# Kernel tuning notes

Measured on AMD Instinct MI355X. Metric: run time of the kernel, lower is better.

Reference implementation:

```python
import jax, jax.numpy as jnp
import numpy as np

B, N, D = 8, 1024, 256
H = 8
DH = D // H
R = 4          # relation types 0..3; adj value 4 = no relation
FF = 1024
EPS = 1e-5


def _lin(k, fan_in, shape):
    return jax.random.normal(k, shape, jnp.float32) * (1.0 / np.sqrt(fan_in))


def setup_inputs() -> dict:
    key = jax.random.key(0)
    ks = jax.random.split(key, 16)
    src = jax.random.normal(ks[0], (B, N, D), jnp.float32)
    adj_matrix = jax.random.randint(ks[1], (B, N, N), 0, 5, dtype=jnp.int32)
    Wq = _lin(ks[2], D, (D, D)); bq = jnp.zeros((D,), jnp.float32)
    Wk = _lin(ks[3], D, (D, D)); bk = jnp.zeros((D,), jnp.float32)
    Wv = _lin(ks[4], D, (R, D, D)); bv = jnp.zeros((R, D), jnp.float32)
    Wo = _lin(ks[5], D, (D, D)); bo = jnp.zeros((D,), jnp.float32)
    W1 = _lin(ks[6], D, (D, FF)); b1 = jnp.zeros((FF,), jnp.float32)
    W2 = _lin(ks[7], FF, (FF, D)); b2 = jnp.zeros((D,), jnp.float32)
    g1 = jnp.ones((D,), jnp.float32); beta1 = jnp.zeros((D,), jnp.float32)
    g2 = jnp.ones((D,), jnp.float32); beta2 = jnp.zeros((D,), jnp.float32)
    return dict(src=src, adj_matrix=adj_matrix, Wq=Wq, bq=bq, Wk=Wk, bk=bk,
                Wv=Wv, bv=bv, Wo=Wo, bo=bo, W1=W1, b1=b1, W2=W2, b2=b2,
                g1=g1, beta1=beta1, g2=g2, beta2=beta2)


def _ln(x, g, b):
    m = x.mean(-1, keepdims=True)
    v = ((x - m) ** 2).mean(-1, keepdims=True)
    return (x - m) * jax.lax.rsqrt(v + EPS) * g + b


def reference(src, adj_matrix, Wq, bq, Wk, bk, Wv, bv, Wo, bo, W1, b1, W2, b2, g1, beta1, g2, beta2):
    Bb, Nn, Dm = src.shape
    h, dh = H, Dm // H
    q = (src @ Wq + bq).reshape(Bb, Nn, h, dh).transpose(0, 2, 1, 3)  # (B,H,N,dh)
    k = (src @ Wk + bk).reshape(Bb, Nn, h, dh).transpose(0, 2, 1, 3)
    scores = jnp.einsum('bhid,bhjd->bhij', q, k) / np.sqrt(dh)
    attn = jax.nn.softmax(scores, axis=-1)                             # (B,H,N,N)
    out = jnp.zeros_like(q)
    for r in range(Wv.shape[0]):  # small fixed relation loop, matches module
        v_r = (src @ Wv[r] + bv[r]).reshape(Bb, Nn, h, dh).transpose(0, 2, 1, 3)
        mask = (adj_matrix == r)[:, None]                              # (B,1,N,N)
        out = out + jnp.einsum('bhij,bhjd->bhid', attn * mask, v_r)
    attn_out = out.transpose(0, 2, 1, 3).reshape(Bb, Nn, Dm) @ Wo + bo
    x = _ln(src + attn_out, g1, beta1)
    ff = jax.nn.gelu(x @ W1 + b1, approximate=False) @ W2 + b2
    return _ln(x + ff, g2, beta2)
```

## Files before the change

### kernel.cpp

```cpp
#include <hip/hip_runtime.h>
#include <hip/hip_bf16.h>
#include <cmath>

constexpr int CB  = 8;
constexpr int CN  = 1024;
constexpr int CD  = 256;
constexpr int CH  = 8;
constexpr int CDH = 32;
constexpr int CR  = 4;
constexpr int CFF = 1024;
constexpr float CEPS = 1e-5f;
constexpr size_t SZH = (size_t)CB * CH * CN * CDH;

#define MODE_QKV   0
#define MODE_OPROJ 1
#define MODE_FFN1  2
#define MODE_FFN2  3

typedef float v4f __attribute__((ext_vector_type(4)));
typedef short v8s __attribute__((ext_vector_type(8)));

static __device__ __forceinline__ short f2bf(float f) {
    unsigned u = __builtin_bit_cast(unsigned, f);
    u += 0x7fff + ((u >> 16) & 1);
    return (short)(u >> 16);
}

static __device__ __forceinline__ void async_copy16(const void* g, void* l) {
    __builtin_amdgcn_global_load_lds(
        (const __attribute__((address_space(1))) void*)g,
        (__attribute__((address_space(3))) void*)l, 16, 0, 0);
}

template<int BM, int BN, int MODE>
__global__ __launch_bounds__(256)
void gemm_mfma(const short* __restrict__ A, const short* __restrict__ Bw,
               const float* __restrict__ biasv, const float* __restrict__ add,
               void* __restrict__ dest, int M, int K, int Nw)
{
    constexpr int WTM = BM / 2, WTN = BN / 2;
    constexpr int TM = WTM / 16, TN = WTN / 16;
    __shared__ short As[2][BM * 32];
    __shared__ short Bs[2][BN * 32];

    const int t    = threadIdx.x;
    const int lane = t & 63;
    const int w    = t >> 6;
    const int quad = lane >> 4, l15 = lane & 15;
    const int wm = w >> 1, wn = w & 1;
    const int m0 = blockIdx.x * BM, n0 = blockIdx.y * BN;

    const int srow = lane >> 2;
    const int scol = (lane & 3) * 8;

    v4f acc[TM][TN];
    #pragma unroll
    for (int i = 0; i < TM; ++i)
        #pragma unroll
        for (int j = 0; j < TN; ++j) acc[i][j] = (v4f){0.f, 0.f, 0.f, 0.f};

    for (int kt = 0; kt < K; kt += 64) {
        __syncthreads();
        #pragma unroll
        for (int s = 0; s < 2; ++s) {
            #pragma unroll
            for (int u = 0; u < BM / 64; ++u) {
                const int e0 = (w * (BM / 64) + u) * 512;
                const int row = (e0 >> 5) + srow;
                async_copy16(A + (size_t)(m0 + row) * K + kt + s * 32 + scol, &As[s][e0]);
            }
            #pragma unroll
            for (int u = 0; u < BN / 64; ++u) {
                const int e0 = (w * (BN / 64) + u) * 512;
                const int row = (e0 >> 5) + srow;
                async_copy16(Bw + (size_t)(n0 + row) * K + kt + s * 32 + scol, &Bs[s][e0]);
            }
        }
        __syncthreads();

        #pragma unroll
        for (int s = 0; s < 2; ++s) {
            v8s af[TM], bfr[TN];
            #pragma unroll
            for (int i = 0; i < TM; ++i)
                af[i] = *(const v8s*)&As[s][(wm * WTM + i * 16 + l15) * 32 + quad * 8];
            #pragma unroll
            for (int j = 0; j < TN; ++j)
                bfr[j] = *(const v8s*)&Bs[s][(wn * WTN + j * 16 + l15) * 32 + quad * 8];
            #pragma unroll
            for (int i = 0; i < TM; ++i)
                #pragma unroll
                for (int j = 0; j < TN; ++j)
                    acc[i][j] = __builtin_amdgcn_mfma_f32_16x16x32_bf16(
                        af[i], bfr[j], acc[i][j], 0, 0, 0);
        }
    }

    #pragma unroll
    for (int i = 0; i < TM; ++i) {
        #pragma unroll
        for (int j = 0; j < TN; ++j) {
            const int mb = m0 + wm * WTM + i * 16 + quad * 4;
            const int n  = n0 + wn * WTN + j * 16 + l15;
            float vals[4];
            #pragma unroll
            for (int rr = 0; rr < 4; ++rr) vals[rr] = acc[i][j][rr] + biasv[n];

            if (MODE == MODE_QKV) {
                const int b = mb >> 10, ii0 = mb & 1023;
                if (n < 512) {
                    const int plane = n >> 8, nn = n & 255;
                    const int h = nn >> 5, d = nn & 31;
                    #pragma unroll
                    for (int rr = 0; rr < 4; ++rr)
                        ((short*)dest)[(size_t)plane * SZH +
                            (((size_t)(b * CH + h)) * CN + ii0 + rr) * CDH + d] =
                            f2bf(vals[rr]);
                } else {
                    const int r2 = (n - 512) >> 8, nn = (n - 512) & 255;
                    const int h = nn >> 5, d = nn & 31;
                    short4 sv;
                    sv.x = f2bf(vals[0]); sv.y = f2bf(vals[1]);
                    sv.z = f2bf(vals[2]); sv.w = f2bf(vals[3]);
                    *(short4*)&((short*)dest)[2 * SZH +
                        (((size_t)(r2 * 64 + b * CH + h)) * CDH + d) * CN + ii0] = sv;
                }
            } else if (MODE == MODE_OPROJ || MODE == MODE_FFN2) {
                #pragma unroll
                for (int rr = 0; rr < 4; ++rr) {
                    const size_t idx = (size_t)(mb + rr) * Nw + n;
                    ((float*)dest)[idx] = vals[rr] + add[idx];
                }
            } else {
                #pragma unroll
                for (int rr = 0; rr < 4; ++rr) {
                    const size_t idx = (size_t)(mb + rr) * Nw + n;
                    ((short*)dest)[idx] = f2bf(0.5f * vals[rr] *
                        (1.0f + erff(vals[rr] * 0.70710678118654752f)));
                }
            }
        }
    }
}

__global__ __launch_bounds__(256)
void prep(const int* __restrict__ adj, const float* __restrict__ src,
          const float* __restrict__ Wq, const float* __restrict__ Wk,
          const float* __restrict__ Wv, const float* __restrict__ Wo,
          const float* __restrict__ W1, const float* __restrict__ W2,
          const float* __restrict__ bq, const float* __restrict__ bk,
          const float* __restrict__ bv, const float* __restrict__ bo,
          const float* __restrict__ b1, const float* __restrict__ b2,
          unsigned char* __restrict__ adj8, short* __restrict__ src_bf,
          short* __restrict__ wqkvT, short* __restrict__ woT,
          short* __restrict__ w1T, short* __restrict__ w2T,
          float* __restrict__ bpack)
{
    const int bx = blockIdx.x, t = threadIdx.x;
    if (bx < 8192) {
        const int i = bx * 256 + t;
        const int4 vv = ((const int4*)adj)[i];
        uchar4 c;
        c.x = (unsigned char)vv.x; c.y = (unsigned char)vv.y;
        c.z = (unsigned char)vv.z; c.w = (unsigned char)vv.w;
        ((uchar4*)adj8)[i] = c;
    } else if (bx < 10240) {
        const int i = (bx - 8192) * 256 + t;
        const float4 v = ((const float4*)src)[i];
        short4 o;
        o.x = f2bf(v.x); o.y = f2bf(v.y); o.z = f2bf(v.z); o.w = f2bf(v.w);
        ((short4*)src_bf)[i] = o;
    } else if (bx < 11776) {
        const int idx = (bx - 10240) * 256 + t;
        const int n = idx >> 8, k = idx & 255;
        float v;
        if (n < 256)      v = Wq[k * 256 + n];
        else if (n < 512) v = Wk[k * 256 + (n - 256)];
        else { const int r = (n - 512) >> 8;
               v = Wv[((size_t)r * 256 + k) * 256 + ((n - 512) & 255)]; }
        wqkvT[idx] = f2bf(v);
    } else if (bx < 12032) {
        const int idx = (bx - 11776) * 256 + t;
        const int n = idx >> 8, k = idx & 255;
        woT[idx] = f2bf(Wo[k * 256 + n]);
    } else if (bx < 13056) {
        const int idx = (bx - 12032) * 256 + t;
        const int n = idx >> 8, k = idx & 255;
        w1T[idx] = f2bf(W1[k * 1024 + n]);
    } else if (bx < 14080) {
        const int idx = (bx - 13056) * 256 + t;
        const int n = idx >> 10, k = idx & 1023;
        w2T[idx] = f2bf(W2[k * 256 + n]);
    } else {
        const int idx = (bx - 14080) * 256 + t;
        float bvv;
        if (idx < 256)       bvv = bq[idx];
        else if (idx < 512)  bvv = bk[idx - 256];
        else if (idx < 1536) bvv = bv[idx - 512];
        else if (idx < 1792) bvv = bo[idx - 1536];
        else if (idx < 2816) bvv = b1[idx - 1792];
        else                 bvv = b2[idx - 2816];
        bpack[idx] = bvv;
    }
}

__global__ __launch_bounds__(256)
void attn_mfma(const short* __restrict__ qg, const short* __restrict__ kg,
               const short* __restrict__ vt, const unsigned char* __restrict__ adj8,
               short* __restrict__ outh)
{
    __shared__ __align__(16) short ks[64 * 32];
    __shared__ __align__(16) short vtile[4][32][72];
    __shared__ __align__(16) short ps[64][68];
    __shared__ __align__(16) unsigned char adjs[64][72];
    __shared__ int lut[64][4];

    const int t    = threadIdx.x;
    const int lane = t & 63;
    const int w    = t >> 6;
    const int quad = lane >> 4;
    const int l15  = lane & 15;
    const int i0   = blockIdx.x * 64;
    const int h    = blockIdx.y;
    const int b    = blockIdx.z;
    const int bhh  = b * CH + h;
    const size_t bh = (size_t)bhh;

    if (t < 64) {
        const int b0 = t & 7, b1 = t >> 3;
        #pragma unroll
        for (int r = 0; r < 4; ++r) {
            const int lo = (b0 == r) ? 0x0100 : 0x0c0c;
            const int hi = (b1 == r) ? 0x0302 : 0x0c0c;
            lut[t][r] = lo | (hi << 16);
        }
    }

    const v8s qfrag = *(const v8s*)&qg[(bh * CN + i0 + 16 * w + l15) * CDH + quad * 8];

    v4f oacc[2];
    oacc[0] = (v4f){0.f, 0.f, 0.f, 0.f};
    oacc[1] = (v4f){0.f, 0.f, 0.f, 0.f};
    float plsum[4] = {0.f, 0.f, 0.f, 0.f};

    const float cs = 0.25503480f;
    const int arow = 16 * w + l15;

    const int srow = lane >> 2;
    const int scol = (lane & 3) * 8;
    const int vd0  = lane >> 3;
    const int vc   = (lane & 7) * 8;
    const short* vplane = vt + (((size_t)(w * 64 + bhh)) * CDH) * CN;
    const int aro = t >> 2;
    const int aco = (t & 3) * 16;

    for (int jt = 0; jt < 16; ++jt) {
        const int j0 = jt * 64;
        __syncthreads();

        async_copy16(kg + (bh * CN + j0 + 16 * w + srow) * CDH + scol,
                     &ks[(16 * w + srow) * 32]);
        #pragma unroll
        for (int it = 0; it < 4; ++it) {
            const int d = vd0 + 8 * it;
            const v8s vv = *(const v8s*)&vplane[(size_t)d * CN + j0 + vc];
            *(v8s*)&vtile[w][d][vc] = vv;
        }
        const int4 av = *(const int4*)&adj8[((size_t)b * CN + i0 + aro) * CN + j0 + aco];
        *(int4*)&adjs[aro][aco] = av;
        __syncthreads();

        v4f sacc[4];
        #pragma unroll
        for (int jb = 0; jb < 4; ++jb) {
            const v8s kfrag = *(const v8s*)&ks[(16 * jb + l15) * 32 + quad * 8];
            sacc[jb] = __builtin_amdgcn_mfma_f32_16x16x32_bf16(
                qfrag, kfrag, (v4f){0.f, 0.f, 0.f, 0.f}, 0, 0, 0);
        }

        #pragma unroll
        for (int rr = 0; rr < 4; ++rr) {
            const int prow = 16 * w + quad * 4 + rr;
            float p[4];
            #pragma unroll
            for (int jb = 0; jb < 4; ++jb) p[jb] = exp2f(cs * sacc[jb][rr]);
            plsum[rr] += (p[0] + p[1]) + (p[2] + p[3]);
            #pragma unroll
            for (int jb = 0; jb < 4; ++jb)
                ps[prow][16 * jb + l15] = f2bf(p[jb]);
        }

        #pragma unroll
        for (int kb = 0; kb < 2; ++kb) {
            const int2 p0 = *(const int2*)&ps[arow][32 * kb + quad * 8];
            const int2 p1 = *(const int2*)&ps[arow][32 * kb + quad * 8 + 4];
            const int2 ab = *(const int2*)&adjs[arow][32 * kb + quad * 8];
            int pf[4][4];
            #pragma unroll
            for (int half = 0; half < 2; ++half) {
                const unsigned a = (unsigned)(half ? ab.y : ab.x);
                const int P0 = half ? p1.x : p0.x;
                const int P1 = half ? p1.y : p0.y;
                const int idxA = (a & 7) | ((a >> 5) & 0x38);
                const int idxB = ((a >> 16) & 7) | ((a >> 21) & 0x38);
                const int4 selA = *(const int4*)&lut[idxA][0];
                const int4 selB = *(const int4*)&lut[idxB][0];
                pf[0][half * 2 + 0] = __builtin_amdgcn_perm(P0, P0, selA.x);
                pf[1][half * 2 + 0] = __builtin_amdgcn_perm(P0, P0, selA.y);
                pf[2][half * 2 + 0] = __builtin_amdgcn_perm(P0, P0, selA.z);
                pf[3][half * 2 + 0] = __builtin_amdgcn_perm(P0, P0, selA.w);
                pf[0][half * 2 + 1] = __builtin_amdgcn_perm(P1, P1, selB.x);
                pf[1][half * 2 + 1] = __builtin_amdgcn_perm(P1, P1, selB.y);
                pf[2][half * 2 + 1] = __builtin_amdgcn_perm(P1, P1, selB.z);
                pf[3][half * 2 + 1] = __builtin_amdgcn_perm(P1, P1, selB.w);
            }
            #pragma unroll
            for (int r = 0; r < 4; ++r) {
                const v8s pfr = __builtin_bit_cast(v8s,
                    make_int4(pf[r][0], pf[r][1], pf[r][2], pf[r][3]));
                #pragma unroll
                for (int cb = 0; cb < 2; ++cb) {
                    const v8s vfrag = *(const v8s*)&vtile[r][16 * cb + l15][32 * kb + quad * 8];
                    oacc[cb] = __builtin_amdgcn_mfma_f32_16x16x32_bf16(
                        pfr, vfrag, oacc[cb], 0, 0, 0);
                }
            }
        }
    }

    #pragma unroll
    for (int rr = 0; rr < 4; ++rr) {
        float l = plsum[rr];
        #pragma unroll
        for (int off = 1; off < 16; off <<= 1) l += __shfl_xor(l, off);
        const float inv = 1.f / l;
        const int row = i0 + 16 * w + quad * 4 + rr;
        #pragma unroll
        for (int cb = 0; cb < 2; ++cb)
            outh[((size_t)b * CN + row) * CD + h * CDH + 16 * cb + l15] =
                f2bf(oacc[cb][rr] * inv);
    }
}

__global__ __launch_bounds__(256)
void ln_kernel(const float* __restrict__ in, const float* __restrict__ g,
               const float* __restrict__ be, float* __restrict__ out,
               short* __restrict__ outb)
{
    __shared__ float red[4];
    const int row = blockIdx.x;
    const int t = threadIdx.x;
    const float x = in[(size_t)row * CD + t];

    float s = x;
    #pragma unroll
    for (int off = 32; off > 0; off >>= 1) s += __shfl_xor(s, off);
    if ((t & 63) == 0) red[t >> 6] = s;
    __syncthreads();
    const float mean = (red[0] + red[1] + red[2] + red[3]) * (1.f / CD);
    __syncthreads();

    const float dx = x - mean;
    float s2 = dx * dx;
    #pragma unroll
    for (int off = 32; off > 0; off >>= 1) s2 += __shfl_xor(s2, off);
    if ((t & 63) == 0) red[t >> 6] = s2;
    __syncthreads();
    const float var = (red[0] + red[1] + red[2] + red[3]) * (1.f / CD);

    const float y = dx * rsqrtf(var + CEPS) * g[t] + be[t];
    out[(size_t)row * CD + t] = y;
    if (outb) outb[(size_t)row * CD + t] = f2bf(y);
}

extern "C" void kernel_launch(void* const* d_in, const int* in_sizes, int n_in,
                              void* d_out, int out_size, void* d_ws, size_t ws_size,
                              hipStream_t stream)
{
    const float* src = (const float*)d_in[0];
    const int*   adj = (const int*)d_in[1];
    const float* Wq  = (const float*)d_in[2];
    const float* bq  = (const float*)d_in[3];
    const float* Wk  = (const float*)d_in[4];
    const float* bk  = (const float*)d_in[5];
    const float* Wv  = (const float*)d_in[6];
    const float* bv  = (const float*)d_in[7];
    const float* Wo  = (const float*)d_in[8];
    const float* bo  = (const float*)d_in[9];
    const float* W1  = (const float*)d_in[10];
    const float* b1  = (const float*)d_in[11];
    const float* W2  = (const float*)d_in[12];
    const float* b2  = (const float*)d_in[13];
    const float* g1  = (const float*)d_in[14];
    const float* be1 = (const float*)d_in[15];
    const float* g2  = (const float*)d_in[16];
    const float* be2 = (const float*)d_in[17];
    float* out = (float*)d_out;

    char* wsb = (char*)d_ws;
    const size_t MB = (size_t)1 << 20;

    unsigned char* adj8 = (unsigned char*)(wsb);
    short* qkv_bf = (short*)(wsb + 8 * MB);
    short* src_bf = (short*)(wsb + 32 * MB);
    short* wqkvT  = (short*)(wsb + 36 * MB);
    short* woT    = (short*)(wsb + 36 * MB + 768 * 1024);
    short* w1T    = (short*)(wsb + 36 * MB + 896 * 1024);
    short* w2T    = (short*)(wsb + 36 * MB + 1408 * 1024);
    float* bpack  = (float*)(wsb + 36 * MB + 1920 * 1024);
    short* heads_bf = (short*)(wsb + 38 * MB);
    float* tmp1   = (float*)(wsb + 42 * MB);
    float* xres   = (float*)(wsb + 8 * MB);
    short* x_bf   = (short*)(wsb + 32 * MB);
    short* h1_bf  = (short*)(wsb + 16 * MB);
    float* tmp2   = tmp1;

    const int M = CB * CN;
    dim3 blk(256);

    prep<<<dim3(14092), blk, 0, stream>>>(adj, src, Wq, Wk, Wv, Wo, W1, W2,
        bq, bk, bv, bo, b1, b2, adj8, src_bf, wqkvT, woT, w1T, w2T, bpack);

    gemm_mfma<128, 128, MODE_QKV><<<dim3(M / 128, 1536 / 128), blk, 0, stream>>>(
        src_bf, wqkvT, bpack, nullptr, qkv_bf, M, CD, 1536);

    attn_mfma<<<dim3(CN / 64, CH, CB), blk, 0, stream>>>(
        qkv_bf, qkv_bf + SZH, qkv_bf + 2 * SZH, adj8, heads_bf);

    gemm_mfma<128, 64, MODE_OPROJ><<<dim3(M / 128, CD / 64), blk, 0, stream>>>(
        heads_bf, woT, bpack + 1536, src, tmp1, M, CD, CD);
    ln_kernel<<<dim3(M), blk, 0, stream>>>(tmp1, g1, be1, xres, x_bf);

    gemm_mfma<128, 128, MODE_FFN1><<<dim3(M / 128, CFF / 128), blk, 0, stream>>>(
        x_bf, w1T, bpack + 1792, nullptr, h1_bf, M, CD, CFF);
    gemm_mfma<128, 64, MODE_FFN2><<<dim3(M / 128, CD / 64), blk, 0, stream>>>(
        h1_bf, w2T, bpack + 2816, xres, tmp2, M, CFF, CD);
    ln_kernel<<<dim3(M), blk, 0, stream>>>(tmp2, g2, be2, out, nullptr);
}
```

Measured before the change: 256.2 us.

## Double-buffer GEMM K-loop and split V projection into transposed GEMM

```diff
diff --git a/kernel.cpp b/kernel.cpp
--- a/kernel.cpp
+++ b/kernel.cpp
@@ -12,10 +12,11 @@
 constexpr float CEPS = 1e-5f;
 constexpr size_t SZH = (size_t)CB * CH * CN * CDH;
 
-#define MODE_QKV   0
+#define MODE_QK    0
 #define MODE_OPROJ 1
 #define MODE_FFN1  2
 #define MODE_FFN2  3
+#define MODE_VT    4
 
 typedef float v4f __attribute__((ext_vector_type(4)));
 typedef short v8s __attribute__((ext_vector_type(8)));
@@ -59,41 +60,43 @@
         #pragma unroll
         for (int j = 0; j < TN; ++j) acc[i][j] = (v4f){0.f, 0.f, 0.f, 0.f};
 
-    for (int kt = 0; kt < K; kt += 64) {
+    const int NK = K >> 5;
+
+    auto stage = [&](int buf, int kt) {
+        #pragma unroll
+        for (int u = 0; u < BM / 64; ++u) {
+            const int e0 = (w * (BM / 64) + u) * 512;
+            const int row = (e0 >> 5) + srow;
+            async_copy16(A + (size_t)(m0 + row) * K + kt + scol, &As[buf][e0]);
+        }
+        #pragma unroll
+        for (int u = 0; u < BN / 64; ++u) {
+            const int e0 = (w * (BN / 64) + u) * 512;
+            const int row = (e0 >> 5) + srow;
+            async_copy16(Bw + (size_t)(n0 + row) * K + kt + scol, &Bs[buf][e0]);
+        }
+    };
+
+    stage(0, 0);
+
+    for (int it = 0; it < NK; ++it) {
         __syncthreads();
-        #pragma unroll
-        for (int s = 0; s < 2; ++s) {
-            #pragma unroll
-            for (int u = 0; u < BM / 64; ++u) {
-                const int e0 = (w * (BM / 64) + u) * 512;
-                const int row = (e0 >> 5) + srow;
-                async_copy16(A + (size_t)(m0 + row) * K + kt + s * 32 + scol, &As[s][e0]);
-            }
-            #pragma unroll
-            for (int u = 0; u < BN / 64; ++u) {
-                const int e0 = (w * (BN / 64) + u) * 512;
-                const int row = (e0 >> 5) + srow;
-                async_copy16(Bw + (size_t)(n0 + row) * K + kt + s * 32 + scol, &Bs[s][e0]);
-            }
-        }
-        __syncthreads();
-
-        #pragma unroll
-        for (int s = 0; s < 2; ++s) {
-            v8s af[TM], bfr[TN];
-            #pragma unroll
-            for (int i = 0; i < TM; ++i)
-                af[i] = *(const v8s*)&As[s][(wm * WTM + i * 16 + l15) * 32 + quad * 8];
+        if (it + 1 < NK) stage((it + 1) & 1, (it + 1) << 5);
+
+        const int buf = it & 1;
+        v8s af[TM], bfr[TN];
+        #pragma unroll
+        for (int i = 0; i < TM; ++i)
+            af[i] = *(const v8s*)&As[buf][(wm * WTM + i * 16 + l15) * 32 + quad * 8];
+        #pragma unroll
+        for (int j = 0; j < TN; ++j)
+            bfr[j] = *(const v8s*)&Bs[buf][(wn * WTN + j * 16 + l15) * 32 + quad * 8];
+        #pragma unroll
+        for (int i = 0; i < TM; ++i)
             #pragma unroll
             for (int j = 0; j < TN; ++j)
-                bfr[j] = *(const v8s*)&Bs[s][(wn * WTN + j * 16 + l15) * 32 + quad * 8];
-            #pragma unroll
-            for (int i = 0; i < TM; ++i)
-                #pragma unroll
-                for (int j = 0; j < TN; ++j)
-                    acc[i][j] = __builtin_amdgcn_mfma_f32_16x16x32_bf16(
-                        af[i], bfr[j], acc[i][j], 0, 0, 0);
-        }
+                acc[i][j] = __builtin_amdgcn_mfma_f32_16x16x32_bf16(
+                    af[i], bfr[j], acc[i][j], 0, 0, 0);
     }
 
     #pragma unroll
@@ -103,27 +106,33 @@
             const int mb = m0 + wm * WTM + i * 16 + quad * 4;
             const int n  = n0 + wn * WTN + j * 16 + l15;
             float vals[4];
-            #pragma unroll
-            for (int rr = 0; rr < 4; ++rr) vals[rr] = acc[i][j][rr] + biasv[n];
-
-            if (MODE == MODE_QKV) {
+            if (MODE == MODE_VT) {
+                #pragma unroll
+                for (int rr = 0; rr < 4; ++rr) vals[rr] = acc[i][j][rr] + biasv[mb + rr];
+            } else {
+                #pragma unroll
+                for (int rr = 0; rr < 4; ++rr) vals[rr] = acc[i][j][rr] + biasv[n];
+            }
+
+            if (MODE == MODE_QK) {
                 const int b = mb >> 10, ii0 = mb & 1023;
-                if (n < 512) {
-                    const int plane = n >> 8, nn = n & 255;
-                    const int h = nn >> 5, d = nn & 31;
-                    #pragma unroll
-                    for (int rr = 0; rr < 4; ++rr)
-                        ((short*)dest)[(size_t)plane * SZH +
-                            (((size_t)(b * CH + h)) * CN + ii0 + rr) * CDH + d] =
-                            f2bf(vals[rr]);
-                } else {
-                    const int r2 = (n - 512) >> 8, nn = (n - 512) & 255;
-                    const int h = nn >> 5, d = nn & 31;
-                    short4 sv;
-                    sv.x = f2bf(vals[0]); sv.y = f2bf(vals[1]);
-                    sv.z = f2bf(vals[2]); sv.w = f2bf(vals[3]);
-                    *(short4*)&((short*)dest)[2 * SZH +
-                        (((size_t)(r2 * 64 + b * CH + h)) * CDH + d) * CN + ii0] = sv;
+                const int plane = n >> 8, nn = n & 255;
+                const int h = nn >> 5, d = nn & 31;
+                #pragma unroll
+                for (int rr = 0; rr < 4; ++rr)
+                    ((short*)dest)[(size_t)plane * SZH +
+                        (((size_t)(b * CH + h)) * CN + ii0 + rr) * CDH + d] =
+                        f2bf(vals[rr]);
+            } else if (MODE == MODE_VT) {
+                const int b = n >> 10, ii = n & 1023;
+                #pragma unroll
+                for (int rr = 0; rr < 4; ++rr) {
+                    const int m = mb + rr;
+                    const int r2 = m >> 8, hd = m & 255;
+                    const int h = hd >> 5, d = hd & 31;
+                    ((short*)dest)[2 * SZH +
+                        (((size_t)(r2 * 64 + b * CH + h)) * CDH + d) * CN + ii] =
+                        f2bf(vals[rr]);
                 }
             } else if (MODE == MODE_OPROJ || MODE == MODE_FFN2) {
                 #pragma unroll
@@ -421,8 +430,10 @@
     prep<<<dim3(14092), blk, 0, stream>>>(adj, src, Wq, Wk, Wv, Wo, W1, W2,
         bq, bk, bv, bo, b1, b2, adj8, src_bf, wqkvT, woT, w1T, w2T, bpack);
 
-    gemm_mfma<128, 128, MODE_QKV><<<dim3(M / 128, 1536 / 128), blk, 0, stream>>>(
-        src_bf, wqkvT, bpack, nullptr, qkv_bf, M, CD, 1536);
+    gemm_mfma<128, 128, MODE_QK><<<dim3(M / 128, 4), blk, 0, stream>>>(
+        src_bf, wqkvT, bpack, nullptr, qkv_bf, M, CD, 512);
+    gemm_mfma<128, 128, MODE_VT><<<dim3(1024 / 128, M / 128), blk, 0, stream>>>(
+        wqkvT + 512 * 256, src_bf, bpack + 512, nullptr, qkv_bf, 1024, CD, M);
 
     attn_mfma<<<dim3(CN / 64, CH, CB), blk, 0, stream>>>(
         qkv_bf, qkv_bf + SZH, qkv_bf + 2 * SZH, adj8, heads_bf);
```

Result: slower. 262.7 us (+2.6%).
